# Optimization experiments

Hardware: AMD Instinct MI355X
Metric: run time of the kernel (lower is better)

Reference implementation:

```python
import jax, jax.numpy as jnp
import numpy as np

B, T, H = 4, 2048, 512
HEADS = 8
D = H // HEADS  # head dim = 64


def setup_inputs() -> dict:
    key = jax.random.key(0)
    ks = jax.random.split(key, 5)
    s = 1.0 / np.sqrt(H)
    return {
        "x": jax.random.normal(ks[0], (B, T, H), dtype=jnp.float32),
        "w_qkv": jax.random.uniform(ks[1], (H, 3 * H), dtype=jnp.float32, minval=-s, maxval=s),
        "b_qkv": jax.random.uniform(ks[2], (3 * H,), dtype=jnp.float32, minval=-s, maxval=s),
        "w_proj": jax.random.uniform(ks[3], (H, H), dtype=jnp.float32, minval=-s, maxval=s),
        "b_proj": jax.random.uniform(ks[4], (H,), dtype=jnp.float32, minval=-s, maxval=s),
    }


def reference(x, w_qkv, b_qkv, w_proj, b_proj):
    b, t, h = x.shape
    scale = (h // HEADS) ** (-0.5)
    qkv = (x @ w_qkv + b_qkv).reshape(b, t, 3, HEADS, h // HEADS)
    q, k, v = qkv[:, :, 0], qkv[:, :, 1], qkv[:, :, 2]  # [b,t,heads,d]
    q = q * scale
    scores = jnp.einsum('bthd,bThd->bhtT', q, k)  # [b,heads,t,t]
    weights = jax.nn.softmax(scores, axis=-1)
    attn = jnp.einsum('bhtT,bThd->bthd', weights, v).reshape(b, t, h)
    return attn @ w_proj + b_proj
```

## Files before the change

kernel.cpp:

```cpp
#include <hip/hip_runtime.h>
#include <stdint.h>

typedef unsigned short u16;
typedef __attribute__((ext_vector_type(8))) __bf16 bf16x8;
typedef __attribute__((ext_vector_type(4))) __bf16 bf16x4;
typedef __attribute__((ext_vector_type(4))) float f32x4;
typedef __attribute__((ext_vector_type(2))) unsigned int u32x2;
typedef __attribute__((ext_vector_type(4))) unsigned int u32x4;

#define QSCALE 0.18033688011112042f

__device__ __forceinline__ u16 f2bf(float f) {
    uint32_t u = __builtin_bit_cast(uint32_t, f);
    u = (u + 0x7fffu + ((u >> 16) & 1u)) >> 16;
    return (u16)u;
}

__device__ __forceinline__ void gl_lds16(const u16* g, u16* l) {
    __builtin_amdgcn_global_load_lds(
        (__attribute__((address_space(1))) uint32_t*)(g),
        (__attribute__((address_space(3))) uint32_t*)(l), 16, 0, 0);
}

__global__ __launch_bounds__(256) void prep_k(const float* __restrict__ xf,
                                              u16* __restrict__ xbf,
                                              const float* __restrict__ wq,
                                              u16* __restrict__ wqkvT) {
    __shared__ u16 t[64][65];
    const int b = blockIdx.x;
    const int tid = threadIdx.x;
    if (b < 4096) {
        const size_t v = (size_t)b * 256 + tid;
        const f32x4 val = ((const f32x4*)xf)[v];
        u32x2 p;
        p.x = (uint32_t)f2bf(val.x) | ((uint32_t)f2bf(val.y) << 16);
        p.y = (uint32_t)f2bf(val.z) | ((uint32_t)f2bf(val.w) << 16);
        *(u32x2*)&xbf[v * 4] = p;
    } else {
        const int bb = b - 4096;
        const int bx = (bb % 24) << 6, by = (bb / 24) << 6;
        const int tx = tid & 63, ty = tid >> 6;
#pragma unroll
        for (int i = ty; i < 64; i += 4)
            t[i][tx] = f2bf(wq[(size_t)(by + i) * 1536 + bx + tx]);
        __syncthreads();
#pragma unroll
        for (int i = ty; i < 64; i += 4)
            wqkvT[(size_t)(bx + i) * 512 + by + tx] = t[tx][i];
    }
}

__global__ void transpose_cvt_k(const float* __restrict__ in,
                                u16* __restrict__ out, int R, int C) {
    __shared__ u16 t[64][65];
    const int bx = blockIdx.x << 6, by = blockIdx.y << 6;
    const int tx = threadIdx.x, ty = threadIdx.y;
#pragma unroll
    for (int i = ty; i < 64; i += 8)
        t[i][tx] = f2bf(in[(size_t)(by + i) * C + bx + tx]);
    __syncthreads();
#pragma unroll
    for (int i = ty; i < 64; i += 8) out[(size_t)(bx + i) * R + by + tx] = t[tx][i];
}

template <int EPI, int BN>
__global__ __launch_bounds__(256, 3) void gemm_bt_k(
    const u16* __restrict__ A, const u16* __restrict__ Bt,
    const float* __restrict__ bias,
    u16* __restrict__ Qb, u16* __restrict__ Kb, u16* __restrict__ Vt,
    float* __restrict__ OutF) {
    constexpr int MI = (BN == 128) ? 4 : 2;
    constexpr int SSTG = 2 * 128 * 32 + 2 * BN * 32;
    constexpr int SEPI = (EPI == 0) ? 128 * 136 : 0;
    constexpr int SMEM = SSTG > SEPI ? SSTG : SEPI;
    __shared__ u16 smem[SMEM];
    u16* lA = smem;
    u16* lB = smem + 2 * 128 * 32;

    const int tid = threadIdx.x;
    const int w = tid >> 6, l = tid & 63, quad = l >> 4, r = l & 15;
    const int tm = blockIdx.x << 7;
    const int tn = blockIdx.y * BN;
    const int wm = (BN == 128) ? ((w >> 1) << 6) : (w << 5);
    const int wn = (BN == 128) ? ((w & 1) << 6) : 0;
    const int srow = l >> 2, sch = (l & 3) << 3;

    f32x4 acc[MI][4];
#pragma unroll
    for (int i = 0; i < MI; ++i)
#pragma unroll
        for (int j = 0; j < 4; ++j) acc[i][j] = (f32x4){0.f, 0.f, 0.f, 0.f};

    auto stage = [&](int b, int kk) {
#pragma unroll
        for (int ii = 0; ii < 2; ++ii) {
            const int rowl = w * 32 + ii * 16;
            gl_lds16(A + (size_t)(tm + rowl + srow) * 512 + kk + sch,
                     &lA[b * 4096 + rowl * 32]);
        }
        if (BN == 128) {
#pragma unroll
            for (int ii = 0; ii < 2; ++ii) {
                const int rowl = w * 32 + ii * 16;
                gl_lds16(Bt + (size_t)(tn + rowl + srow) * 512 + kk + sch,
                         &lB[b * BN * 32 + rowl * 32]);
            }
        } else {
            const int rowl = w * 16;
            gl_lds16(Bt + (size_t)(tn + rowl + srow) * 512 + kk + sch,
                     &lB[b * BN * 32 + rowl * 32]);
        }
    };

    stage(0, 0);
    __syncthreads();

    int cur = 0;
    for (int kk = 0; kk < 512; kk += 32) {
        if (kk + 32 < 512) stage(cur ^ 1, kk + 32);
        bf16x8 af[MI], bfr[4];
#pragma unroll
        for (int mi = 0; mi < MI; ++mi)
            af[mi] =
                *(const bf16x8*)&lA[cur * 4096 + (wm + mi * 16 + r) * 32 + quad * 8];
#pragma unroll
        for (int ni = 0; ni < 4; ++ni)
            bfr[ni] =
                *(const bf16x8*)&lB[cur * BN * 32 + (wn + ni * 16 + r) * 32 + quad * 8];
#pragma unroll
        for (int mi = 0; mi < MI; ++mi)
#pragma unroll
            for (int ni = 0; ni < 4; ++ni)
                acc[mi][ni] = __builtin_amdgcn_mfma_f32_16x16x32_bf16(
                    af[mi], bfr[ni], acc[mi][ni], 0, 0, 0);
        __syncthreads();
        cur ^= 1;
    }

    if (EPI == 1) {
#pragma unroll
        for (int ni = 0; ni < 4; ++ni) {
            const int n = tn + wn + ni * 16 + r;
            const float bv = bias[n];
#pragma unroll
            for (int mi = 0; mi < MI; ++mi)
#pragma unroll
                for (int i = 0; i < 4; ++i) {
                    const int m = tm + wm + mi * 16 + quad * 4 + i;
                    OutF[(size_t)m * 512 + n] = acc[mi][ni][i] + bv;
                }
        }
    } else {
        const bool isV = (tn >= 1024);
        const bool isQ = (tn < 512);
#pragma unroll
        for (int ni = 0; ni < 4; ++ni) {
            const int nl = wn + ni * 16 + r;
            const float bv = bias[tn + nl];
#pragma unroll
            for (int mi = 0; mi < MI; ++mi)
#pragma unroll
                for (int i = 0; i < 4; ++i) {
                    const int ml = wm + mi * 16 + quad * 4 + i;
                    float v = acc[mi][ni][i] + bv;
                    if (isQ) v *= QSCALE;
                    const u16 hb = f2bf(v);
                    if (isV)
                        smem[nl * 136 + ml] = hb;
                    else
                        smem[ml * 136 + nl] = hb;
                }
        }
        __syncthreads();
        const int tbb = tm >> 11, tt = tm & 2047;
        if (!isV) {
            u16* base = isQ ? Qb : Kb;
            const int mlr = l >> 3, ls = l & 7;
#pragma unroll
            for (int rg = 0; rg < 4; ++rg)
#pragma unroll
                for (int h = 0; h < 2; ++h) {
                    const int ml = (w * 4 + rg) * 8 + mlr;
                    const int head = ((tn + h * 64) >> 6) & 7;
                    const int bh = tbb * 8 + head;
                    const u32x4 dv = *(const u32x4*)&smem[ml * 136 + h * 64 + ls * 8];
                    *(u32x4*)&base[((size_t)(bh * 2048 + tt + ml) << 6) + ls * 8] = dv;
                }
        } else {
            const int nlr = l >> 4, ls = l & 15;
#pragma unroll
            for (int j2 = 0; j2 < 8; ++j2) {
                const int nl = w * 32 + j2 * 4 + nlr;
                const int n = tn + nl;
                const int d = n & 63, head = (n >> 6) & 7;
                const int bh = tbb * 8 + head;
                const u32x4 dv = *(const u32x4*)&smem[nl * 136 + ls * 8];
                *(u32x4*)&Vt[((size_t)(bh * 64 + d) << 11) + tt + ls * 8] = dv;
            }
        }
    }
}

__global__ __launch_bounds__(256, 2) void attn_k(
    const u16* __restrict__ Qb, const u16* __restrict__ Kb,
    const u16* __restrict__ Vt, u16* __restrict__ attnb) {
    __shared__ u16 lk[2][64 * 64];
    __shared__ u16 lv[2][64 * 64];
    const int tid = threadIdx.x;
    const int w = tid >> 6, l = tid & 63, quad = l >> 4, r = l & 15;
    const int qt = blockIdx.x, bh = blockIdx.y;
    const size_t qbase = (size_t)bh * 2048 + qt * 128;
    const int srl = l >> 3;
    const int sg = (l & 7) ^ srl;

    const int rl = r & 7;
    const int rhi = r >> 3;
    const int skq = (r & 3) ^ (((r >> 2) & 1) << 1) ^ (((r >> 2) & 2) << 1);
    const int g0 = (quad ^ skq) << 3;

    bf16x8 qf[2][2];
#pragma unroll
    for (int qs = 0; qs < 2; ++qs)
#pragma unroll
        for (int hf = 0; hf < 2; ++hf)
            qf[qs][hf] = *(const bf16x8*)&Qb[((qbase + w * 32 + qs * 16 + r) << 6) +
                                            hf * 32 + quad * 8];

    const u32x4 onesu = {0x3F803F80u, 0x3F803F80u, 0x3F803F80u, 0x3F803F80u};
    const bf16x8 vones = __builtin_bit_cast(bf16x8, onesu);

    f32x4 o[2][4];
#pragma unroll
    for (int qs = 0; qs < 2; ++qs)
#pragma unroll
        for (int i = 0; i < 4; ++i) o[qs][i] = (f32x4){0.f, 0.f, 0.f, 0.f};
    f32x4 osum[2];
    osum[0] = (f32x4){0.f, 0.f, 0.f, 0.f};
    osum[1] = (f32x4){0.f, 0.f, 0.f, 0.f};

    auto stage = [&](int b, int kv0) {
#pragma unroll
        for (int ii = 0; ii < 2; ++ii) {
            const int chunk = w * 2 + ii;
            const int skr = (srl & 3) ^ ((chunk & 1) << 1) ^ ((chunk & 2) << 1);
            gl_lds16(Kb + ((size_t)(bh * 2048 + kv0 + chunk * 8 + srl) << 6) +
                         ((l & 7) ^ skr) * 8,
                     &lk[b][chunk * 512]);
            gl_lds16(Vt + (((size_t)(bh * 64 + chunk * 8 + srl)) << 11) + kv0 + sg * 8,
                     &lv[b][chunk * 512]);
        }
    };

    stage(0, 0);
    __syncthreads();

    int cur = 0;
    for (int kv0 = 0; kv0 < 2048; kv0 += 64) {
        if (kv0 + 64 < 2048) stage(cur ^ 1, kv0 + 64);

        bf16x8 ka[4], kb[4];
#pragma unroll
        for (int kt = 0; kt < 4; ++kt) {
            const int R = (kt & 1) * 32 + (r >> 2) * 8 + (kt >> 1) * 4 + (r & 3);
            ka[kt] = *(const bf16x8*)&lk[cur][R * 64 + g0];
            kb[kt] = *(const bf16x8*)&lk[cur][(R * 64 + g0) ^ 32];
        }
        bf16x8 vb[2][4];
#pragma unroll
        for (int h = 0; h < 2; ++h)
#pragma unroll
            for (int dt = 0; dt < 4; ++dt) {
                const int baseV = (dt * 2 + rhi) * 512 + rl * 64;
                vb[h][dt] = *(const bf16x8*)&lv[cur][baseV + ((h * 4 + quad) ^ rl) * 8];
            }

        bf16x4 pk4[2][4];
#pragma unroll
        for (int kt = 0; kt < 4; ++kt) {
#pragma unroll
            for (int qs = 0; qs < 2; ++qs) {
                f32x4 z = (f32x4){0.f, 0.f, 0.f, 0.f};
                __builtin_amdgcn_s_setprio(1);
                z = __builtin_amdgcn_mfma_f32_16x16x32_bf16(ka[kt], qf[qs][0], z, 0, 0, 0);
                z = __builtin_amdgcn_mfma_f32_16x16x32_bf16(kb[kt], qf[qs][1], z, 0, 0, 0);
                __builtin_amdgcn_s_setprio(0);
                bf16x4 pb;
                pb[0] = (__bf16)__builtin_amdgcn_exp2f(z[0]);
                pb[1] = (__bf16)__builtin_amdgcn_exp2f(z[1]);
                pb[2] = (__bf16)__builtin_amdgcn_exp2f(z[2]);
                pb[3] = (__bf16)__builtin_amdgcn_exp2f(z[3]);
                pk4[qs][kt] = pb;
            }
        }

        __builtin_amdgcn_s_setprio(1);
#pragma unroll
        for (int h = 0; h < 2; ++h) {
            const bf16x8 ap0 = __builtin_shufflevector(pk4[0][h], pk4[0][h + 2],
                                                       0, 1, 2, 3, 4, 5, 6, 7);
            const bf16x8 ap1 = __builtin_shufflevector(pk4[1][h], pk4[1][h + 2],
                                                       0, 1, 2, 3, 4, 5, 6, 7);
#pragma unroll
            for (int dt = 0; dt < 4; ++dt) {
                o[0][dt] = __builtin_amdgcn_mfma_f32_16x16x32_bf16(ap0, vb[h][dt],
                                                                  o[0][dt], 0, 0, 0);
                o[1][dt] = __builtin_amdgcn_mfma_f32_16x16x32_bf16(ap1, vb[h][dt],
                                                                  o[1][dt], 0, 0, 0);
            }
            osum[0] = __builtin_amdgcn_mfma_f32_16x16x32_bf16(ap0, vones, osum[0], 0, 0, 0);
            osum[1] = __builtin_amdgcn_mfma_f32_16x16x32_bf16(ap1, vones, osum[1], 0, 0, 0);
        }
        __builtin_amdgcn_s_setprio(0);

        __syncthreads();
        cur ^= 1;
    }

    const int bb = bh >> 3, head = bh & 7;
#pragma unroll
    for (int qs = 0; qs < 2; ++qs) {
#pragma unroll
        for (int i = 0; i < 4; ++i) {
            const float inv = __builtin_amdgcn_rcpf(osum[qs][i]);
            const int row = bb * 2048 + qt * 128 + w * 32 + qs * 16 + quad * 4 + i;
#pragma unroll
            for (int dt = 0; dt < 4; ++dt)
                attnb[(size_t)row * 512 + head * 64 + dt * 16 + r] =
                    f2bf(o[qs][dt][i] * inv);
        }
    }
}

extern "C" void kernel_launch(void* const* d_in, const int* in_sizes, int n_in,
                              void* d_out, int out_size, void* d_ws, size_t ws_size,
                              hipStream_t stream) {
    const float *x = nullptr, *wq = nullptr, *bq = nullptr, *wp = nullptr, *bp = nullptr;
    for (int i = 0; i < n_in; ++i) {
        switch (in_sizes[i]) {
            case 4194304: x  = (const float*)d_in[i]; break;
            case 786432:  wq = (const float*)d_in[i]; break;
            case 1536:    bq = (const float*)d_in[i]; break;
            case 262144:  wp = (const float*)d_in[i]; break;
            case 512:     bp = (const float*)d_in[i]; break;
        }
    }
    if (!x || !wq || !bq || !wp || !bp) {
        x = (const float*)d_in[0]; wq = (const float*)d_in[1];
        bq = (const float*)d_in[2]; wp = (const float*)d_in[3];
        bp = (const float*)d_in[4];
    }
    float* out = (float*)d_out;

    char* ws = (char*)d_ws;
    u16* attnb  = (u16*)(ws + 0);
    u16* wqkvT  = (u16*)(ws + 0);
    u16* Qb     = (u16*)(ws + 8388608);
    u16* wprojT = (u16*)(ws + 8388608);
    u16* Kb     = (u16*)(ws + 16777216);
    u16* Vt     = (u16*)(ws + 25165824);
    u16* xbf    = (u16*)d_out;

    prep_k<<<dim3(4288), 256, 0, stream>>>(x, xbf, wq, wqkvT);
    gemm_bt_k<0, 128><<<dim3(64, 12), 256, 0, stream>>>(xbf, wqkvT, bq, Qb, Kb, Vt,
                                                        nullptr);
    attn_k<<<dim3(16, 32), 256, 0, stream>>>(Qb, Kb, Vt, attnb);
    transpose_cvt_k<<<dim3(8, 8), dim3(64, 8), 0, stream>>>(wp, wprojT, 512, 512);
    gemm_bt_k<1, 64><<<dim3(64, 8), 256, 0, stream>>>(attnb, wprojT, bp, nullptr,
                                                      nullptr, nullptr, out);
}
```

Measured before the change: 157.6 us.

## Triple-buffer K/V LDS tiles and prefetch next K fragments into registers

Grows the K and V shared-memory staging from two buffers to three, so global loads are issued two tiles ahead. The next tile's K fragments are read from LDS into registers during the PV MFMA phase, with the loop unrolled by two to alternate register sets. This targets load latency and the LDS-read stall before the QK MFMAs. In exchange it uses more LDS (48KB per block) and more VGPRs, which could cut occupancy under the launch bound of 2 blocks per CU.

```diff
diff --git a/kernel.cpp b/kernel.cpp
--- a/kernel.cpp
+++ b/kernel.cpp
@@ -204,8 +204,8 @@
 __global__ __launch_bounds__(256, 2) void attn_k(
     const u16* __restrict__ Qb, const u16* __restrict__ Kb,
     const u16* __restrict__ Vt, u16* __restrict__ attnb) {
-    __shared__ u16 lk[2][64 * 64];
-    __shared__ u16 lv[2][64 * 64];
+    __shared__ u16 lk[3][64 * 64];
+    __shared__ u16 lv[3][64 * 64];
     const int tid = threadIdx.x;
     const int w = tid >> 6, l = tid & 63, quad = l >> 4, r = l & 15;
     const int qt = blockIdx.x, bh = blockIdx.y;
@@ -251,20 +251,34 @@
         }
     };
 
+    int Roff[4];
+#pragma unroll
+    for (int kt = 0; kt < 4; ++kt) {
+        const int R = (kt & 1) * 32 + (r >> 2) * 8 + (kt >> 1) * 4 + (r & 3);
+        Roff[kt] = R * 64 + g0;
+    }
+
+    auto readK = [&](int b, bf16x8 (&ka)[4], bf16x8 (&kb)[4]) {
+        const u16* base = &lk[b][0];
+#pragma unroll
+        for (int kt = 0; kt < 4; ++kt) {
+            ka[kt] = *(const bf16x8*)&base[Roff[kt]];
+            kb[kt] = *(const bf16x8*)&base[Roff[kt] ^ 32];
+        }
+    };
+
     stage(0, 0);
+    stage(1, 64);
     __syncthreads();
 
-    int cur = 0;
-    for (int kv0 = 0; kv0 < 2048; kv0 += 64) {
-        if (kv0 + 64 < 2048) stage(cur ^ 1, kv0 + 64);
-
-        bf16x8 ka[4], kb[4];
-#pragma unroll
-        for (int kt = 0; kt < 4; ++kt) {
-            const int R = (kt & 1) * 32 + (r >> 2) * 8 + (kt >> 1) * 4 + (r & 3);
-            ka[kt] = *(const bf16x8*)&lk[cur][R * 64 + g0];
-            kb[kt] = *(const bf16x8*)&lk[cur][(R * 64 + g0) ^ 32];
-        }
+    bf16x8 kaE[4], kbE[4], kaO[4], kbO[4];
+    readK(0, kaE, kbE);
+
+    int cur = 0, nx1 = 1, nx2 = 2;
+
+    auto body = [&](int t, bf16x8 (&kaP)[4], bf16x8 (&kbP)[4],
+                    bf16x8 (&kaN)[4], bf16x8 (&kbN)[4]) {
+        if (t + 2 < 32) stage(nx2, (t + 2) * 64);
         bf16x8 vb[2][4];
 #pragma unroll
         for (int h = 0; h < 2; ++h)
@@ -273,7 +287,6 @@
                 const int baseV = (dt * 2 + rhi) * 512 + rl * 64;
                 vb[h][dt] = *(const bf16x8*)&lv[cur][baseV + ((h * 4 + quad) ^ rl) * 8];
             }
-
         bf16x4 pk4[2][4];
 #pragma unroll
         for (int kt = 0; kt < 4; ++kt) {
@@ -281,8 +294,8 @@
             for (int qs = 0; qs < 2; ++qs) {
                 f32x4 z = (f32x4){0.f, 0.f, 0.f, 0.f};
                 __builtin_amdgcn_s_setprio(1);
-                z = __builtin_amdgcn_mfma_f32_16x16x32_bf16(ka[kt], qf[qs][0], z, 0, 0, 0);
-                z = __builtin_amdgcn_mfma_f32_16x16x32_bf16(kb[kt], qf[qs][1], z, 0, 0, 0);
+                z = __builtin_amdgcn_mfma_f32_16x16x32_bf16(kaP[kt], qf[qs][0], z, 0, 0, 0);
+                z = __builtin_amdgcn_mfma_f32_16x16x32_bf16(kbP[kt], qf[qs][1], z, 0, 0, 0);
                 __builtin_amdgcn_s_setprio(0);
                 bf16x4 pb;
                 pb[0] = (__bf16)__builtin_amdgcn_exp2f(z[0]);
@@ -292,7 +305,7 @@
                 pk4[qs][kt] = pb;
             }
         }
-
+        if (t + 1 < 32) readK(nx1, kaN, kbN);
         __builtin_amdgcn_s_setprio(1);
 #pragma unroll
         for (int h = 0; h < 2; ++h) {
@@ -313,7 +326,15 @@
         __builtin_amdgcn_s_setprio(0);
 
         __syncthreads();
-        cur ^= 1;
+        const int tmp = cur;
+        cur = nx1;
+        nx1 = nx2;
+        nx2 = tmp;
+    };
+
+    for (int t = 0; t < 32; t += 2) {
+        body(t, kaE, kbE, kaO, kbO);
+        body(t + 1, kaO, kbO, kaE, kbE);
     }
 
     const int bb = bh >> 3, head = bh & 7;
```

Measured after the change: 153.3 us. -2.8%, faster.
